# Kernel tuning notes

Hardware: AMD Instinct MI355X
Metric: run time of the kernel (lower is better)

## Reference

```python
import jax, jax.numpy as jnp
import numpy as np

GROUPS = 8
NEG_SLOPE = 0.1
EPS = 1e-5


def group_norm(x, gamma, beta):
    # x: (B, N, C). Matches torch GroupNorm applied on (B, C, N):
    # normalize over (channels-in-group, N) per batch per group.
    B, N, C = x.shape
    xg = x.reshape(B, N, GROUPS, C // GROUPS)
    mean = xg.mean(axis=(1, 3), keepdims=True)
    var = xg.var(axis=(1, 3), keepdims=True)
    xg = (xg - mean) * jax.lax.rsqrt(var + EPS)
    return xg.reshape(B, N, C) * gamma + beta


def unary_block(x, W, b, gamma, beta):
    # Linear -> GroupNorm -> LeakyReLU(0.1)
    h = jnp.einsum('bnc,cd->bnd', x, W) + b
    h = group_norm(h, gamma, beta)
    return jnp.where(h >= 0, h, NEG_SLOPE * h)


def setup_inputs() -> dict:
    key = jax.random.key(0)
    ks = jax.random.split(key, 16)
    B, N, M, K, Cin, Cout = 4, 8192, 32768, 16, 128, 128
    inp = {
        'q_feats': jax.random.normal(ks[0], (B, N, Cin), jnp.float32),
        's_feats': jax.random.normal(ks[1], (B, M, Cin), jnp.float32),
        'q_points': jax.random.normal(ks[2], (B, N, 3), jnp.float32),
        's_points': jax.random.normal(ks[3], (B, N, K, 3), jnp.float32),
        'downsample_indices': jax.random.randint(ks[4], (B, N, K), 0, M, jnp.int32),
    }
    sc1 = 1.0 / np.sqrt(Cin)
    sc2 = 1.0 / np.sqrt(Cout)
    inp['W1'] = jax.random.uniform(ks[5], (Cin, Cout), jnp.float32, -sc1, sc1)
    inp['b1'] = jnp.zeros((Cout,), jnp.float32)
    inp['g1'] = jnp.ones((Cout,), jnp.float32)
    inp['be1'] = jnp.zeros((Cout,), jnp.float32)
    inp['W2'] = jax.random.uniform(ks[6], (Cout, Cout), jnp.float32, -sc2, sc2)
    inp['b2'] = jnp.zeros((Cout,), jnp.float32)
    inp['g2'] = jnp.ones((Cout,), jnp.float32)
    inp['be2'] = jnp.zeros((Cout,), jnp.float32)
    inp['W3'] = jax.random.uniform(ks[7], (Cout, Cout), jnp.float32, -sc2, sc2)
    inp['b3'] = jnp.zeros((Cout,), jnp.float32)
    inp['g3'] = jnp.ones((Cout,), jnp.float32)
    inp['be3'] = jnp.zeros((Cout,), jnp.float32)
    return inp


def reference(q_feats, s_feats, q_points, s_points, downsample_indices,
              W1, b1, g1, be1, W2, b2, g2, be2, W3, b3, g3, be3):
    # knn_gather: (B, N, K, C) gathered from (B, M, C)
    grouped = jax.vmap(lambda f, i: f[i])(s_feats, downsample_indices)
    # inverse-squared-distance weights over K neighbors
    d2 = jnp.sum((s_points - q_points[:, :, None, :]) ** 2, axis=-1)  # (B,N,K)
    w = 1.0 / (d2 + 1e-8)
    w = w / jnp.sum(w, axis=-1, keepdims=True)
    latent = jnp.sum(grouped * w[..., None], axis=2)  # (B,N,C)
    h = unary_block(latent, W1, b1, g1, be1)
    h = unary_block(h, W2, b2, g2, be2)
    return unary_block(h + q_feats, W3, b3, g3, be3)
```

## Files before the change

### kernel.cpp

```cpp
#include <hip/hip_runtime.h>


constexpr int NPB = 8192;
constexpr int BN  = 32768;
constexpr int CH  = 128;
constexpr int KNB = 16;
constexpr int MS  = 32768;
constexpr int NG  = 8;
constexpr int CG  = 16;
constexpr int RPB = 64;
constexpr int NBLK = BN / RPB;
constexpr int BPB  = NPB / RPB;
constexpr int XS = 144;
constexpr int WS = 144;

typedef short short8 __attribute__((ext_vector_type(8)));
typedef float floatx4 __attribute__((ext_vector_type(4)));

__device__ __forceinline__ unsigned short f2bs(float f) {
    unsigned int u = __builtin_bit_cast(unsigned int, f);
    unsigned int r = (u + 0x7fffu + ((u >> 16) & 1u)) >> 16;
    return (unsigned short)r;
}
__device__ __forceinline__ float bs2f(unsigned short s) {
    unsigned int u = ((unsigned int)s) << 16;
    return __builtin_bit_cast(float, u);
}

__global__ __launch_bounds__(256) void k_prep(
    const float* __restrict__ W1, const float* __restrict__ W2,
    const float* __restrict__ W3,
    unsigned short* __restrict__ Wt1, unsigned short* __restrict__ Wt2,
    unsigned short* __restrict__ Wt3)
{
    const int bi = blockIdx.x;
    const int w  = bi >> 6;
    const int i  = bi & 63;
    const int el = i * 256 + threadIdx.x;
    const int n  = el >> 7, k = el & 127;
    const float* W = (w == 0) ? W1 : (w == 1) ? W2 : W3;
    unsigned short* Wt = (w == 0) ? Wt1 : (w == 1) ? Wt2 : Wt3;
    Wt[n * 128 + k] = f2bs(W[k * 128 + n]);
}

template <int MODE>
__global__ __launch_bounds__(256) void k_pass(
    const unsigned short* __restrict__ hin,
    const float* __restrict__ part_in,
    const float* __restrict__ gamma,
    const float* __restrict__ beta,
    const float* __restrict__ qf,
    const float* __restrict__ sf,
    const float* __restrict__ qp,
    const float* __restrict__ sp,
    const int*   __restrict__ idx,
    const unsigned short* __restrict__ Wt,
    const float* __restrict__ bias,
    unsigned short* __restrict__ hout,
    float* __restrict__ part_out)
{
    const int bi = blockIdx.x;
    const int t  = threadIdx.x;
    const int b  = bi / BPB;

    __shared__ unsigned short Xl[RPB * XS];
    __shared__ unsigned short Wl[CH * WS];
    __shared__ float red[16][17];
    __shared__ float2 stats_s[NG];
    __shared__ float wv[RPB * KNB];
    __shared__ float winv[RPB];
    __shared__ float pw[4][16];

    #pragma unroll
    for (int i = 0; i < 8; i++) {
        int el = i * 2048 + t * 8;
        short8 w8 = *(const short8*)(Wt + el);
        *(short8*)&Wl[(el >> 7) * WS + (el & 127)] = w8;
    }

    if (MODE == 0) {
        #pragma unroll
        for (int i = 0; i < 4; i++) {
            int p = i * 256 + t;
            int row = p >> 4, k = p & 15;
            size_t rg = (size_t)bi * RPB + row;
            float qx = qp[rg * 3 + 0], qy = qp[rg * 3 + 1], qz = qp[rg * 3 + 2];
            const float* spp = sp + (rg * KNB + k) * 3;
            float dx = spp[0] - qx, dy = spp[1] - qy, dz = spp[2] - qz;
            wv[p] = 1.0f / (dx * dx + dy * dy + dz * dz + 1e-8f);
        }
        __syncthreads();
        if (t < RPB) {
            float s = 0.f;
            #pragma unroll
            for (int k = 0; k < KNB; k++) s += wv[t * KNB + k];
            winv[t] = 1.0f / s;
        }
        __syncthreads();
        const int grp = t >> 5, c4 = (t & 31) * 4;
        for (int rr = 0; rr < 8; rr++) {
            int row = grp * 8 + rr;
            size_t rg = (size_t)bi * RPB + row;
            const int* ip = idx + rg * KNB;
            float ax = 0.f, ay = 0.f, az = 0.f, aw = 0.f;
            #pragma unroll
            for (int k = 0; k < KNB; k++) {
                int j = ip[k];
                const float4 f = *(const float4*)(sf + ((size_t)b * MS + j) * CH + c4);
                float w = wv[row * KNB + k];
                ax += w * f.x; ay += w * f.y; az += w * f.z; aw += w * f.w;
            }
            float wi = winv[row];
            ushort4 pk;
            pk.x = f2bs(ax * wi); pk.y = f2bs(ay * wi);
            pk.z = f2bs(az * wi); pk.w = f2bs(aw * wi);
            *(ushort4*)&Xl[row * XS + c4] = pk;
        }
    } else {
        {
            int j = t & 15, chunk = t >> 4;
            float acc = 0.f;
            #pragma unroll
            for (int i = 0; i < 8; i++)
                acc += part_in[(size_t)(b * BPB + chunk * 8 + i) * 16 + j];
            red[chunk][j] = acc;
        }
        __syncthreads();
        if (t < NG) {
            float s = 0.f, q = 0.f;
            #pragma unroll
            for (int c = 0; c < 16; c++) { s += red[c][t]; q += red[c][t + 8]; }
            const float cnt = (float)(NPB * CG);
            float mean = s / cnt;
            float var  = q / cnt - mean * mean;
            stats_s[t] = make_float2(mean, rsqrtf(var + 1e-5f));
        }
        __syncthreads();
        #pragma unroll
        for (int i = 0; i < 4; i++) {
            int flat = i * 2048 + t * 8;
            int row = flat >> 7, col = flat & 127;
            size_t gidx = (size_t)bi * RPB * CH + flat;
            short8 hv = *(const short8*)(hin + gidx);
            float2 st = stats_s[col >> 4];
            float4 g0 = *(const float4*)(gamma + col);
            float4 g1 = *(const float4*)(gamma + col + 4);
            float4 b0 = *(const float4*)(beta + col);
            float4 b1 = *(const float4*)(beta + col + 4);
            float gg[8] = {g0.x, g0.y, g0.z, g0.w, g1.x, g1.y, g1.z, g1.w};
            float bb[8] = {b0.x, b0.y, b0.z, b0.w, b1.x, b1.y, b1.z, b1.w};
            float re[8];
            if (MODE == 2) {
                float4 r0 = *(const float4*)(qf + gidx);
                float4 r1 = *(const float4*)(qf + gidx + 4);
                re[0]=r0.x; re[1]=r0.y; re[2]=r0.z; re[3]=r0.w;
                re[4]=r1.x; re[5]=r1.y; re[6]=r1.z; re[7]=r1.w;
            }
            unsigned short ov[8];
            #pragma unroll
            for (int e = 0; e < 8; e++) {
                float v = bs2f((unsigned short)hv[e]);
                float y = (v - st.x) * st.y * gg[e] + bb[e];
                y = (y >= 0.f) ? y : 0.1f * y;
                if (MODE == 2) y += re[e];
                ov[e] = f2bs(y);
            }
            *(short8*)&Xl[row * XS + col] = *(short8*)ov;
        }
    }
    __syncthreads();

    const int w  = t >> 6;
    const int l  = t & 63;
    const int lr = l & 15;
    const int qd = l >> 4;
    floatx4 acc[8] = {};
    #pragma unroll
    for (int kt = 0; kt < 4; kt++) {
        short8 a = *(const short8*)&Xl[(w * 16 + lr) * XS + kt * 32 + qd * 8];
        #pragma unroll
        for (int j = 0; j < 8; j++) {
            short8 bf = *(const short8*)&Wl[(j * 16 + lr) * WS + kt * 32 + qd * 8];
            acc[j] = __builtin_amdgcn_mfma_f32_16x16x32_bf16(a, bf, acc[j], 0, 0, 0);
        }
    }

    float vals[8][4];
    #pragma unroll
    for (int j = 0; j < 8; j++) {
        float bj = bias[j * 16 + lr];
        float ss = 0.f, qq = 0.f;
        #pragma unroll
        for (int r = 0; r < 4; r++) {
            float v = acc[j][r] + bj;
            vals[j][r] = v;
            ss += v; qq += v * v;
        }
        #pragma unroll
        for (int off = 32; off; off >>= 1) {
            ss += __shfl_down(ss, off);
            qq += __shfl_down(qq, off);
        }
        if (l == 0) { pw[w][j] = ss; pw[w][8 + j] = qq; }
    }
    #pragma unroll
    for (int j = 0; j < 8; j++)
        #pragma unroll
        for (int r = 0; r < 4; r++)
            Xl[(w * 16 + qd * 4 + r) * XS + j * 16 + lr] = f2bs(vals[j][r]);
    __syncthreads();
    if (t < 16)
        part_out[(size_t)bi * 16 + t] = pw[0][t] + pw[1][t] + pw[2][t] + pw[3][t];
    #pragma unroll
    for (int i = 0; i < 4; i++) {
        int flat = i * 2048 + t * 8;
        int row = flat >> 7, col = flat & 127;
        *(short8*)(hout + (size_t)bi * RPB * CH + flat) =
            *(const short8*)&Xl[row * XS + col];
    }
}

__global__ __launch_bounds__(256) void k_out(
    const unsigned short* __restrict__ hin, const float* __restrict__ part_in,
    const float* __restrict__ gamma, const float* __restrict__ beta,
    float* __restrict__ out)
{
    const int bi = blockIdx.x;
    const int t  = threadIdx.x;
    const int b  = bi / BPB;
    __shared__ float red[16][17];
    __shared__ float2 stats_s[NG];
    {
        int j = t & 15, chunk = t >> 4;
        float acc = 0.f;
        #pragma unroll
        for (int i = 0; i < 8; i++)
            acc += part_in[(size_t)(b * BPB + chunk * 8 + i) * 16 + j];
        red[chunk][j] = acc;
    }
    __syncthreads();
    if (t < NG) {
        float s = 0.f, q = 0.f;
        #pragma unroll
        for (int c = 0; c < 16; c++) { s += red[c][t]; q += red[c][t + 8]; }
        const float cnt = (float)(NPB * CG);
        float mean = s / cnt;
        float var  = q / cnt - mean * mean;
        stats_s[t] = make_float2(mean, rsqrtf(var + 1e-5f));
    }
    __syncthreads();
    #pragma unroll
    for (int i = 0; i < 4; i++) {
        int flat = i * 2048 + t * 8;
        int col = flat & 127;
        size_t gidx = (size_t)bi * RPB * CH + flat;
        short8 hv = *(const short8*)(hin + gidx);
        float2 st = stats_s[col >> 4];
        float4 g0 = *(const float4*)(gamma + col);
        float4 g1 = *(const float4*)(gamma + col + 4);
        float4 b0 = *(const float4*)(beta + col);
        float4 b1 = *(const float4*)(beta + col + 4);
        float gg[8] = {g0.x, g0.y, g0.z, g0.w, g1.x, g1.y, g1.z, g1.w};
        float bb[8] = {b0.x, b0.y, b0.z, b0.w, b1.x, b1.y, b1.z, b1.w};
        float o[8];
        #pragma unroll
        for (int e = 0; e < 8; e++) {
            float v = bs2f((unsigned short)hv[e]);
            float y = (v - st.x) * st.y * gg[e] + bb[e];
            o[e] = (y >= 0.f) ? y : 0.1f * y;
        }
        float4 o0 = {o[0], o[1], o[2], o[3]};
        float4 o1 = {o[4], o[5], o[6], o[7]};
        *(float4*)(out + gidx)     = o0;
        *(float4*)(out + gidx + 4) = o1;
    }
}

extern "C" void kernel_launch(void* const* d_in, const int* in_sizes, int n_in,
                              void* d_out, int out_size, void* d_ws, size_t ws_size,
                              hipStream_t stream) {
    const float* qf  = (const float*)d_in[0];
    const float* sf  = (const float*)d_in[1];
    const float* qp  = (const float*)d_in[2];
    const float* sp  = (const float*)d_in[3];
    const int*   idx = (const int*)  d_in[4];
    const float* W1  = (const float*)d_in[5];
    const float* b1  = (const float*)d_in[6];
    const float* g1  = (const float*)d_in[7];
    const float* be1 = (const float*)d_in[8];
    const float* W2  = (const float*)d_in[9];
    const float* b2  = (const float*)d_in[10];
    const float* g2  = (const float*)d_in[11];
    const float* be2 = (const float*)d_in[12];
    const float* W3  = (const float*)d_in[13];
    const float* b3  = (const float*)d_in[14];
    const float* g3  = (const float*)d_in[15];
    const float* be3 = (const float*)d_in[16];

    char* ws = (char*)d_ws;
    unsigned short* Wt1 = (unsigned short*)(ws);
    unsigned short* Wt2 = (unsigned short*)(ws + 32768);
    unsigned short* Wt3 = (unsigned short*)(ws + 65536);
    float* p1 = (float*)(ws + 98304);
    float* p2 = (float*)(ws + 131072);
    float* p3 = (float*)(ws + 163840);
    unsigned short* h1 = (unsigned short*)(ws + 196608);
    unsigned short* h2 = (unsigned short*)(ws + 196608 + 8388608);
    unsigned short* h3 = (unsigned short*)(ws + 196608 + 2 * 8388608);
    float* out = (float*)d_out;

    k_prep<<<192, 256, 0, stream>>>(W1, W2, W3, Wt1, Wt2, Wt3);
    k_pass<0><<<NBLK, 256, 0, stream>>>(nullptr, nullptr, nullptr, nullptr,
                                        nullptr, sf, qp, sp, idx,
                                        Wt1, b1, h1, p1);
    k_pass<1><<<NBLK, 256, 0, stream>>>(h1, p1, g1, be1, nullptr,
                                        nullptr, nullptr, nullptr, nullptr,
                                        Wt2, b2, h2, p2);
    k_pass<2><<<NBLK, 256, 0, stream>>>(h2, p2, g2, be2, qf,
                                        nullptr, nullptr, nullptr, nullptr,
                                        Wt3, b3, h3, p3);
    k_out<<<NBLK, 256, 0, stream>>>(h3, p3, g3, be3, out);
}
```

Baseline: 196.0 us.

## Halve rows per block, keep weights in registers, hoist group-norm stat reduction

Rows per block drop from 64 to 32, which doubles the block count. Each wave now loads its B-fragments of the weight matrix straight into registers, so the shared-memory copy of W goes away and LDS use shrinks. The per-block reduction of group-norm partials, previously repeated in every block, moves into a small separate k_reduce kernel launched between passes. The gather indices are staged in LDS, the output kernel is simplified, and there are three extra kernel launches.

Result: slower. 206.1 us (+5.2%).

```diff
diff --git a/kernel.cpp b/kernel.cpp
--- a/kernel.cpp
+++ b/kernel.cpp
@@ -8,11 +8,10 @@
 constexpr int MS  = 32768;
 constexpr int NG  = 8;
 constexpr int CG  = 16;
-constexpr int RPB = 64;
+constexpr int RPB = 32;
 constexpr int NBLK = BN / RPB;
 constexpr int BPB  = NPB / RPB;
 constexpr int XS = 144;
-constexpr int WS = 144;
 
 typedef short short8 __attribute__((ext_vector_type(8)));
 typedef float floatx4 __attribute__((ext_vector_type(4)));
@@ -35,18 +34,43 @@
 {
     const int bi = blockIdx.x;
     const int w  = bi >> 6;
-    const int i  = bi & 63;
-    const int el = i * 256 + threadIdx.x;
-    const int n  = el >> 7, k = el & 127;
+    const int el = (bi & 63) * 256 + threadIdx.x;
     const float* W = (w == 0) ? W1 : (w == 1) ? W2 : W3;
     unsigned short* Wt = (w == 0) ? Wt1 : (w == 1) ? Wt2 : Wt3;
-    Wt[n * 128 + k] = f2bs(W[k * 128 + n]);
+    float v = W[el];
+    int k = el >> 7, n = el & 127;
+    Wt[n * 128 + k] = f2bs(v);
+}
+
+__global__ __launch_bounds__(256) void k_reduce(
+    const float* __restrict__ partials, float2* __restrict__ stats)
+{
+    const int bg = blockIdx.x;
+    const int b  = bg >> 3;
+    const int g  = bg & 7;
+    const int t  = threadIdx.x;
+    const float* p = partials + ((size_t)(b * BPB + t)) * 16;
+    float s = p[g];
+    float q = p[8 + g];
+    __shared__ float ss[256], qq[256];
+    ss[t] = s; qq[t] = q;
+    __syncthreads();
+    for (int off = 128; off; off >>= 1) {
+        if (t < off) { ss[t] += ss[t + off]; qq[t] += qq[t + off]; }
+        __syncthreads();
+    }
+    if (t == 0) {
+        const float cnt  = (float)(NPB * CG);
+        float mean = ss[0] / cnt;
+        float var  = qq[0] / cnt - mean * mean;
+        stats[bg] = make_float2(mean, rsqrtf(var + 1e-5f));
+    }
 }
 
 template <int MODE>
-__global__ __launch_bounds__(256) void k_pass(
+__global__ __launch_bounds__(256, 4) void k_pass(
     const unsigned short* __restrict__ hin,
-    const float* __restrict__ part_in,
+    const float2* __restrict__ stats,
     const float* __restrict__ gamma,
     const float* __restrict__ beta,
     const float* __restrict__ qf,
@@ -61,26 +85,31 @@
 {
     const int bi = blockIdx.x;
     const int t  = threadIdx.x;
-    const int b  = bi / BPB;
+    const int b  = bi >> 8;
+
+    const int w  = t >> 6;
+    const int l  = t & 63;
+    const int lr = l & 15;
+    const int qd = l >> 4;
 
     __shared__ unsigned short Xl[RPB * XS];
-    __shared__ unsigned short Wl[CH * WS];
-    __shared__ float red[16][17];
-    __shared__ float2 stats_s[NG];
     __shared__ float wv[RPB * KNB];
+    __shared__ int   ii[RPB * KNB];
     __shared__ float winv[RPB];
-    __shared__ float pw[4][16];
-
-    #pragma unroll
-    for (int i = 0; i < 8; i++) {
-        int el = i * 2048 + t * 8;
-        short8 w8 = *(const short8*)(Wt + el);
-        *(short8*)&Wl[(el >> 7) * WS + (el & 127)] = w8;
-    }
+    __shared__ float pw[4][4];
+
+    short8 wf[2][4];
+    #pragma unroll
+    for (int jj = 0; jj < 2; jj++)
+        #pragma unroll
+        for (int kt = 0; kt < 4; kt++)
+            wf[jj][kt] = *(const short8*)(Wt + ((2 * w + jj) * 16 + lr) * 128
+                                          + kt * 32 + qd * 8);
+    float bjv[2] = {bias[(2 * w + 0) * 16 + lr], bias[(2 * w + 1) * 16 + lr]};
 
     if (MODE == 0) {
         #pragma unroll
-        for (int i = 0; i < 4; i++) {
+        for (int i = 0; i < 2; i++) {
             int p = i * 256 + t;
             int row = p >> 4, k = p & 15;
             size_t rg = (size_t)bi * RPB + row;
@@ -88,6 +117,7 @@
             const float* spp = sp + (rg * KNB + k) * 3;
             float dx = spp[0] - qx, dy = spp[1] - qy, dz = spp[2] - qz;
             wv[p] = 1.0f / (dx * dx + dy * dy + dz * dz + 1e-8f);
+            ii[p] = idx[rg * KNB + k];
         }
         __syncthreads();
         if (t < RPB) {
@@ -98,17 +128,16 @@
         }
         __syncthreads();
         const int grp = t >> 5, c4 = (t & 31) * 4;
-        for (int rr = 0; rr < 8; rr++) {
-            int row = grp * 8 + rr;
-            size_t rg = (size_t)bi * RPB + row;
-            const int* ip = idx + rg * KNB;
+        #pragma unroll
+        for (int rr = 0; rr < 4; rr++) {
+            int row = grp * 4 + rr;
             float ax = 0.f, ay = 0.f, az = 0.f, aw = 0.f;
             #pragma unroll
             for (int k = 0; k < KNB; k++) {
-                int j = ip[k];
+                int j = ii[row * KNB + k];
                 const float4 f = *(const float4*)(sf + ((size_t)b * MS + j) * CH + c4);
-                float w = wv[row * KNB + k];
-                ax += w * f.x; ay += w * f.y; az += w * f.z; aw += w * f.w;
+                float wk = wv[row * KNB + k];
+                ax += wk * f.x; ay += wk * f.y; az += wk * f.z; aw += wk * f.w;
             }
             float wi = winv[row];
             ushort4 pk;
@@ -117,162 +146,120 @@
             *(ushort4*)&Xl[row * XS + c4] = pk;
         }
     } else {
-        {
-            int j = t & 15, chunk = t >> 4;
-            float acc = 0.f;
+        const int flat = t * 16;
+        const int row = flat >> 7, col = flat & 127;
+        size_t gidx = (size_t)bi * RPB * CH + flat;
+        short8 h0 = *(const short8*)(hin + gidx);
+        short8 h1 = *(const short8*)(hin + gidx + 8);
+        float2 st = stats[b * NG + (col >> 4)];
+        float gg[16], bb[16], re[16];
+        #pragma unroll
+        for (int e4 = 0; e4 < 4; e4++) {
+            float4 g = *(const float4*)(gamma + col + e4 * 4);
+            float4 bt = *(const float4*)(beta + col + e4 * 4);
+            gg[e4*4+0]=g.x; gg[e4*4+1]=g.y; gg[e4*4+2]=g.z; gg[e4*4+3]=g.w;
+            bb[e4*4+0]=bt.x; bb[e4*4+1]=bt.y; bb[e4*4+2]=bt.z; bb[e4*4+3]=bt.w;
+            if (MODE == 2) {
+                float4 r = *(const float4*)(qf + gidx + e4 * 4);
+                re[e4*4+0]=r.x; re[e4*4+1]=r.y; re[e4*4+2]=r.z; re[e4*4+3]=r.w;
+            }
+        }
+        unsigned short ov[16];
+        #pragma unroll
+        for (int e = 0; e < 16; e++) {
+            unsigned short hs = (unsigned short)((e < 8) ? h0[e] : h1[e - 8]);
+            float v = bs2f(hs);
+            float y = (v - st.x) * st.y * gg[e] + bb[e];
+            y = (y >= 0.f) ? y : 0.1f * y;
+            if (MODE == 2) y += re[e];
+            ov[e] = f2bs(y);
+        }
+        *(short8*)&Xl[row * XS + col]     = *(short8*)&ov[0];
+        *(short8*)&Xl[row * XS + col + 8] = *(short8*)&ov[8];
+    }
+    __syncthreads();
+
+    floatx4 acc[2][2] = {};
+    #pragma unroll
+    for (int kt = 0; kt < 4; kt++) {
+        short8 a0 = *(const short8*)&Xl[lr * XS + kt * 32 + qd * 8];
+        short8 a1 = *(const short8*)&Xl[(16 + lr) * XS + kt * 32 + qd * 8];
+        #pragma unroll
+        for (int jj = 0; jj < 2; jj++) {
+            acc[0][jj] = __builtin_amdgcn_mfma_f32_16x16x32_bf16(a0, wf[jj][kt], acc[0][jj], 0, 0, 0);
+            acc[1][jj] = __builtin_amdgcn_mfma_f32_16x16x32_bf16(a1, wf[jj][kt], acc[1][jj], 0, 0, 0);
+        }
+    }
+
+    #pragma unroll
+    for (int jj = 0; jj < 2; jj++) {
+        float ss = 0.f, qq = 0.f;
+        #pragma unroll
+        for (int m = 0; m < 2; m++)
             #pragma unroll
-            for (int i = 0; i < 8; i++)
-                acc += part_in[(size_t)(b * BPB + chunk * 8 + i) * 16 + j];
-            red[chunk][j] = acc;
-        }
-        __syncthreads();
-        if (t < NG) {
-            float s = 0.f, q = 0.f;
-            #pragma unroll
-            for (int c = 0; c < 16; c++) { s += red[c][t]; q += red[c][t + 8]; }
-            const float cnt = (float)(NPB * CG);
-            float mean = s / cnt;
-            float var  = q / cnt - mean * mean;
-            stats_s[t] = make_float2(mean, rsqrtf(var + 1e-5f));
-        }
-        __syncthreads();
-        #pragma unroll
-        for (int i = 0; i < 4; i++) {
-            int flat = i * 2048 + t * 8;
-            int row = flat >> 7, col = flat & 127;
-            size_t gidx = (size_t)bi * RPB * CH + flat;
-            short8 hv = *(const short8*)(hin + gidx);
-            float2 st = stats_s[col >> 4];
-            float4 g0 = *(const float4*)(gamma + col);
-            float4 g1 = *(const float4*)(gamma + col + 4);
-            float4 b0 = *(const float4*)(beta + col);
-            float4 b1 = *(const float4*)(beta + col + 4);
-            float gg[8] = {g0.x, g0.y, g0.z, g0.w, g1.x, g1.y, g1.z, g1.w};
-            float bb[8] = {b0.x, b0.y, b0.z, b0.w, b1.x, b1.y, b1.z, b1.w};
-            float re[8];
-            if (MODE == 2) {
-                float4 r0 = *(const float4*)(qf + gidx);
-                float4 r1 = *(const float4*)(qf + gidx + 4);
-                re[0]=r0.x; re[1]=r0.y; re[2]=r0.z; re[3]=r0.w;
-                re[4]=r1.x; re[5]=r1.y; re[6]=r1.z; re[7]=r1.w;
+            for (int r = 0; r < 4; r++) {
+                float v = acc[m][jj][r] + bjv[jj];
+                ss += v; qq += v * v;
             }
-            unsigned short ov[8];
-            #pragma unroll
-            for (int e = 0; e < 8; e++) {
-                float v = bs2f((unsigned short)hv[e]);
-                float y = (v - st.x) * st.y * gg[e] + bb[e];
-                y = (y >= 0.f) ? y : 0.1f * y;
-                if (MODE == 2) y += re[e];
-                ov[e] = f2bs(y);
-            }
-            *(short8*)&Xl[row * XS + col] = *(short8*)ov;
-        }
-    }
-    __syncthreads();
-
-    const int w  = t >> 6;
-    const int l  = t & 63;
-    const int lr = l & 15;
-    const int qd = l >> 4;
-    floatx4 acc[8] = {};
-    #pragma unroll
-    for (int kt = 0; kt < 4; kt++) {
-        short8 a = *(const short8*)&Xl[(w * 16 + lr) * XS + kt * 32 + qd * 8];
-        #pragma unroll
-        for (int j = 0; j < 8; j++) {
-            short8 bf = *(const short8*)&Wl[(j * 16 + lr) * WS + kt * 32 + qd * 8];
-            acc[j] = __builtin_amdgcn_mfma_f32_16x16x32_bf16(a, bf, acc[j], 0, 0, 0);
-        }
-    }
-
-    float vals[8][4];
-    #pragma unroll
-    for (int j = 0; j < 8; j++) {
-        float bj = bias[j * 16 + lr];
-        float ss = 0.f, qq = 0.f;
-        #pragma unroll
-        for (int r = 0; r < 4; r++) {
-            float v = acc[j][r] + bj;
-            vals[j][r] = v;
-            ss += v; qq += v * v;
-        }
         #pragma unroll
         for (int off = 32; off; off >>= 1) {
             ss += __shfl_down(ss, off);
             qq += __shfl_down(qq, off);
         }
-        if (l == 0) { pw[w][j] = ss; pw[w][8 + j] = qq; }
-    }
-    #pragma unroll
-    for (int j = 0; j < 8; j++)
-        #pragma unroll
-        for (int r = 0; r < 4; r++)
-            Xl[(w * 16 + qd * 4 + r) * XS + j * 16 + lr] = f2bs(vals[j][r]);
+        if (l == 0) { pw[w][jj] = ss; pw[w][2 + jj] = qq; }
+    }
     __syncthreads();
-    if (t < 16)
-        part_out[(size_t)bi * 16 + t] = pw[0][t] + pw[1][t] + pw[2][t] + pw[3][t];
-    #pragma unroll
-    for (int i = 0; i < 4; i++) {
-        int flat = i * 2048 + t * 8;
-        int row = flat >> 7, col = flat & 127;
-        *(short8*)(hout + (size_t)bi * RPB * CH + flat) =
-            *(const short8*)&Xl[row * XS + col];
+    #pragma unroll
+    for (int jj = 0; jj < 2; jj++)
+        #pragma unroll
+        for (int m = 0; m < 2; m++)
+            #pragma unroll
+            for (int r = 0; r < 4; r++)
+                Xl[(m * 16 + qd * 4 + r) * XS + (2 * w + jj) * 16 + lr] =
+                    f2bs(acc[m][jj][r] + bjv[jj]);
+    __syncthreads();
+    if (t < 16) {
+        int g = t & 7, isq = t >> 3;
+        part_out[(size_t)bi * 16 + t] = pw[g >> 1][(g & 1) + 2 * isq];
+    }
+    {
+        const int flat = t * 16;
+        const int row = flat >> 7, col = flat & 127;
+        size_t gidx = (size_t)bi * RPB * CH + flat;
+        *(short8*)(hout + gidx)     = *(const short8*)&Xl[row * XS + col];
+        *(short8*)(hout + gidx + 8) = *(const short8*)&Xl[row * XS + col + 8];
     }
 }
 
 __global__ __launch_bounds__(256) void k_out(
-    const unsigned short* __restrict__ hin, const float* __restrict__ part_in,
+    const unsigned short* __restrict__ hin, const float2* __restrict__ stats,
     const float* __restrict__ gamma, const float* __restrict__ beta,
     float* __restrict__ out)
 {
-    const int bi = blockIdx.x;
-    const int t  = threadIdx.x;
-    const int b  = bi / BPB;
-    __shared__ float red[16][17];
-    __shared__ float2 stats_s[NG];
-    {
-        int j = t & 15, chunk = t >> 4;
-        float acc = 0.f;
-        #pragma unroll
-        for (int i = 0; i < 8; i++)
-            acc += part_in[(size_t)(b * BPB + chunk * 8 + i) * 16 + j];
-        red[chunk][j] = acc;
-    }
-    __syncthreads();
-    if (t < NG) {
-        float s = 0.f, q = 0.f;
-        #pragma unroll
-        for (int c = 0; c < 16; c++) { s += red[c][t]; q += red[c][t + 8]; }
-        const float cnt = (float)(NPB * CG);
-        float mean = s / cnt;
-        float var  = q / cnt - mean * mean;
-        stats_s[t] = make_float2(mean, rsqrtf(var + 1e-5f));
-    }
-    __syncthreads();
-    #pragma unroll
-    for (int i = 0; i < 4; i++) {
-        int flat = i * 2048 + t * 8;
-        int col = flat & 127;
-        size_t gidx = (size_t)bi * RPB * CH + flat;
-        short8 hv = *(const short8*)(hin + gidx);
-        float2 st = stats_s[col >> 4];
-        float4 g0 = *(const float4*)(gamma + col);
-        float4 g1 = *(const float4*)(gamma + col + 4);
-        float4 b0 = *(const float4*)(beta + col);
-        float4 b1 = *(const float4*)(beta + col + 4);
-        float gg[8] = {g0.x, g0.y, g0.z, g0.w, g1.x, g1.y, g1.z, g1.w};
-        float bb[8] = {b0.x, b0.y, b0.z, b0.w, b1.x, b1.y, b1.z, b1.w};
-        float o[8];
-        #pragma unroll
-        for (int e = 0; e < 8; e++) {
-            float v = bs2f((unsigned short)hv[e]);
-            float y = (v - st.x) * st.y * gg[e] + bb[e];
-            o[e] = (y >= 0.f) ? y : 0.1f * y;
-        }
-        float4 o0 = {o[0], o[1], o[2], o[3]};
-        float4 o1 = {o[4], o[5], o[6], o[7]};
-        *(float4*)(out + gidx)     = o0;
-        *(float4*)(out + gidx + 4) = o1;
+    const int t = threadIdx.x;
+    size_t fl = (size_t)blockIdx.x * 4096 + t * 16;
+    const int b = (int)(fl >> 20);
+    const int col = (int)(fl & 127);
+    short8 h0 = *(const short8*)(hin + fl);
+    short8 h1 = *(const short8*)(hin + fl + 8);
+    float2 st = stats[b * NG + (col >> 4)];
+    #pragma unroll
+    for (int e4 = 0; e4 < 4; e4++) {
+        float4 g = *(const float4*)(gamma + col + e4 * 4);
+        float4 bt = *(const float4*)(beta + col + e4 * 4);
+        float o[4];
+        #pragma unroll
+        for (int i = 0; i < 4; i++) {
+            int e = e4 * 4 + i;
+            unsigned short hs = (unsigned short)((e < 8) ? h0[e] : h1[e - 8]);
+            float v = bs2f(hs);
+            float gv = (i == 0) ? g.x : (i == 1) ? g.y : (i == 2) ? g.z : g.w;
+            float bv = (i == 0) ? bt.x : (i == 1) ? bt.y : (i == 2) ? bt.z : bt.w;
+            float y = (v - st.x) * st.y * gv + bv;
+            o[i] = (y >= 0.f) ? y : 0.1f * y;
+        }
+        float4 ov = {o[0], o[1], o[2], o[3]};
+        *(float4*)(out + fl + e4 * 4) = ov;
     }
 }
 
@@ -301,23 +288,29 @@
     unsigned short* Wt1 = (unsigned short*)(ws);
     unsigned short* Wt2 = (unsigned short*)(ws + 32768);
     unsigned short* Wt3 = (unsigned short*)(ws + 65536);
-    float* p1 = (float*)(ws + 98304);
-    float* p2 = (float*)(ws + 131072);
-    float* p3 = (float*)(ws + 163840);
-    unsigned short* h1 = (unsigned short*)(ws + 196608);
-    unsigned short* h2 = (unsigned short*)(ws + 196608 + 8388608);
-    unsigned short* h3 = (unsigned short*)(ws + 196608 + 2 * 8388608);
+    float*  p1  = (float*)(ws + 98304);
+    float*  p2  = (float*)(ws + 163840);
+    float*  p3  = (float*)(ws + 229376);
+    float2* st1 = (float2*)(ws + 294912);
+    float2* st2 = (float2*)(ws + 295168);
+    float2* st3 = (float2*)(ws + 295424);
+    unsigned short* h1 = (unsigned short*)(ws + 327680);
+    unsigned short* h2 = (unsigned short*)(ws + 327680 + 8388608);
+    unsigned short* h3 = (unsigned short*)(ws + 327680 + 2 * 8388608);
     float* out = (float*)d_out;
 
     k_prep<<<192, 256, 0, stream>>>(W1, W2, W3, Wt1, Wt2, Wt3);
     k_pass<0><<<NBLK, 256, 0, stream>>>(nullptr, nullptr, nullptr, nullptr,
                                         nullptr, sf, qp, sp, idx,
                                         Wt1, b1, h1, p1);
-    k_pass<1><<<NBLK, 256, 0, stream>>>(h1, p1, g1, be1, nullptr,
+    k_reduce<<<32, 256, 0, stream>>>(p1, st1);
+    k_pass<1><<<NBLK, 256, 0, stream>>>(h1, st1, g1, be1, nullptr,
                                         nullptr, nullptr, nullptr, nullptr,
                                         Wt2, b2, h2, p2);
-    k_pass<2><<<NBLK, 256, 0, stream>>>(h2, p2, g2, be2, qf,
+    k_reduce<<<32, 256, 0, stream>>>(p2, st2);
+    k_pass<2><<<NBLK, 256, 0, stream>>>(h2, st2, g2, be2, qf,
                                         nullptr, nullptr, nullptr, nullptr,
                                         Wt3, b3, h3, p3);
-    k_out<<<NBLK, 256, 0, stream>>>(h3, p3, g3, be3, out);
-}
+    k_reduce<<<32, 256, 0, stream>>>(p3, st3);
+    k_out<<<1024, 256, 0, stream>>>(h3, st3, g3, be3, out);
+}
```
